# Optimization experiments

Measured on AMD Instinct MI355X. Metric: run time of the kernel, lower is better.

Reference implementation:

```python
import jax, jax.numpy as jnp
import numpy as np

N_QUBITS = 8
N_QLAYERS = 7
EPS = 1e-12


def _conv(x, w, b, stride, pad):
    y = jax.lax.conv_general_dilated(x, w, (stride, stride), [(pad, pad), (pad, pad)],
                                     dimension_numbers=("NCHW", "OIHW", "NCHW"))
    return y + b[None, :, None, None]


def _adaptive_avg_pool(x, out):
    # torch AdaptiveAvgPool2d semantics: bin i = [floor(i*H/out), ceil((i+1)*H/out))
    H, W = x.shape[-2], x.shape[-1]
    hs = [(i * H) // out for i in range(out)]
    he = [-(-((i + 1) * H) // out) for i in range(out)]
    ws = [(i * W) // out for i in range(out)]
    we = [-(-((i + 1) * W) // out) for i in range(out)]
    xh = jnp.stack([x[:, :, s:e, :].mean(axis=2) for s, e in zip(hs, he)], axis=2)
    return jnp.stack([xh[:, :, :, s:e].mean(axis=3) for s, e in zip(ws, we)], axis=3)


def _ry(st, theta, wire):
    # st: [B, 2, 2, ..., 2]; RY = [[cos, -sin], [sin, cos]] (real)
    c, s = jnp.cos(theta / 2), jnp.sin(theta / 2)
    U = jnp.stack([jnp.stack([c, -s]), jnp.stack([s, c])])  # [2,2]
    m = jnp.moveaxis(st, wire + 1, -1)
    m = m @ U.T
    return jnp.moveaxis(m, -1, wire + 1)


def _cnot(st, ctrl, tgt):
    s = jnp.moveaxis(st, (ctrl + 1, tgt + 1), (1, 2))
    s = jnp.stack([s[:, 0], jnp.flip(s[:, 1], axis=1)], axis=1)
    return jnp.moveaxis(s, (1, 2), (ctrl + 1, tgt + 1))


def _quantum(feat, q_w):
    B = feat.shape[0]
    psi = feat / jnp.maximum(jnp.linalg.norm(feat, axis=1, keepdims=True), EPS)
    st = psi.reshape((B,) + (2,) * N_QUBITS)  # wire 0 = most significant axis
    for l in range(N_QLAYERS):
        for q in range(N_QUBITS):
            st = _ry(st, q_w[l, q], q)
        for q in range(N_QUBITS - 1):
            st = _cnot(st, q, q + 1)
    s2 = st.reshape(B, 2, -1)
    return jnp.sum(s2[:, 0] ** 2, axis=-1) - jnp.sum(s2[:, 1] ** 2, axis=-1)  # [B]


def _forward(x, conv1_w, conv1_b, conv2_w, conv2_b, conv3_w, conv3_b, fc_w, fc_b, q_w,
             c1_w, c1_b, c2_w, c2_b, c3_w, c3_b, c4_w, c4_b, c5_w, c5_b):
    h = jax.nn.relu(_conv(x, conv1_w, conv1_b, 2, 2))   # [B,8,14,14]
    h = jax.nn.relu(_conv(h, conv2_w, conv2_b, 2, 1))   # [B,16,7,7]
    h = jax.nn.relu(_conv(h, conv3_w, conv3_b, 1, 1))   # [B,32,7,7]
    h = _adaptive_avg_pool(h, 3)                         # [B,32,3,3]
    h = h.reshape(h.shape[0], -1)                        # [B,288]
    feat = jax.nn.relu(h @ fc_w.T + fc_b)                # [B,256] (dropout = eval no-op)
    feat = feat / jnp.maximum(jnp.linalg.norm(feat, axis=1, keepdims=True), EPS)
    q = _quantum(feat, q_w)[:, None]                     # [B,1]
    h = jax.nn.relu(q @ c1_w.T + c1_b)
    h = jax.nn.relu(h @ c2_w.T + c2_b)
    h = jax.nn.relu(h @ c3_w.T + c3_b)
    h = jax.nn.relu(h @ c4_w.T + c4_b)
    return jax.nn.sigmoid(h @ c5_w.T + c5_b)             # [B,1]


def setup_inputs() -> dict:
    key = jax.random.key(0)
    ks = jax.random.split(key, 32)
    B = 8192
    def rn(k, shape, scale):
        return jax.random.normal(k, shape, dtype=jnp.float32) * scale
    return {
        "x": rn(ks[0], (B, 1, 28, 28), 1.0),
        "conv1_w": rn(ks[1], (8, 1, 5, 5), 0.2), "conv1_b": rn(ks[2], (8,), 0.05),
        "conv2_w": rn(ks[3], (16, 8, 3, 3), 0.12), "conv2_b": rn(ks[4], (16,), 0.05),
        "conv3_w": rn(ks[5], (32, 16, 3, 3), 0.08), "conv3_b": rn(ks[6], (32,), 0.05),
        "fc_w": rn(ks[7], (256, 288), 0.06), "fc_b": rn(ks[8], (256,), 0.02),
        "q_w": rn(ks[9], (7, 8), 1.0),
        "c1_w": rn(ks[10], (512, 1), 0.5), "c1_b": rn(ks[11], (512,), 0.02),
        "c2_w": rn(ks[12], (256, 512), 0.04), "c2_b": rn(ks[13], (256,), 0.02),
        "c3_w": rn(ks[14], (128, 256), 0.06), "c3_b": rn(ks[15], (128,), 0.02),
        "c4_w": rn(ks[16], (64, 128), 0.09), "c4_b": rn(ks[17], (64,), 0.02),
        "c5_w": rn(ks[18], (1, 64), 0.12), "c5_b": rn(ks[19], (1,), 0.02),
    }


def reference(x, conv1_w, conv1_b, conv2_w, conv2_b, conv3_w, conv3_b, fc_w, fc_b, q_w,
              c1_w, c1_b, c2_w, c2_b, c3_w, c3_b, c4_w, c4_b, c5_w, c5_b):
    return _forward(x, conv1_w, conv1_b, conv2_w, conv2_b, conv3_w, conv3_b, fc_w, fc_b, q_w,
                    c1_w, c1_b, c2_w, c2_b, c3_w, c3_b, c4_w, c4_b, c5_w, c5_b)
```

## Files before the change

kernel.cpp:

```cpp
#include <hip/hip_runtime.h>
#include <math.h>


typedef __attribute__((ext_vector_type(8))) short bf16x8;
typedef __attribute__((ext_vector_type(4))) float f32x4;

__device__ __forceinline__ unsigned rne_bf16(float x) {
  unsigned u = __float_as_uint(x);
  return (u + 0x7FFFu + ((u >> 16) & 1u)) & 0xFFFF0000u;
}

__global__ __launch_bounds__(256) void k_conv12(
    const float* __restrict__ x,
    const float* __restrict__ w1, const float* __restrict__ b1,
    const float* __restrict__ w2, const float* __restrict__ b2,
    float* __restrict__ y2p) {
  __shared__ float xin[4][784];
  __shared__ float y1p[4][8][14][20];
  __shared__ float wl1[200], bl1[8];
  __shared__ float wl2t[72][16], bl2[16];
  const int n0 = blockIdx.x * 4;
  const int tid = threadIdx.x;

  for (int i = tid; i < 200; i += 256) wl1[i] = w1[i];
  if (tid < 8) bl1[tid] = b1[tid];
  for (int i = tid; i < 1152; i += 256) {
    int k = i >> 4, co = i & 15;
    wl2t[k][co] = w2[co * 72 + k];
  }
  if (tid < 16) bl2[tid] = b2[tid];
#pragma unroll
  for (int s = 0; s < 4; ++s)
    if (tid < 196)
      reinterpret_cast<float4*>(&xin[s][0])[tid] =
          reinterpret_cast<const float4*>(&x[(size_t)(n0 + s) * 784])[tid];
  __syncthreads();

  if (tid < 224) {
    const int s = tid / 56, r = tid % 56, co = r / 7, oyh = r % 7;
    float wreg[25];
#pragma unroll
    for (int i = 0; i < 25; ++i) wreg[i] = wl1[co * 25 + i];
    const float bb = bl1[co];
#pragma unroll
    for (int half = 0; half < 2; ++half) {
      const int oy = oyh + half * 7;
      float acc[14];
#pragma unroll
      for (int ox = 0; ox < 14; ++ox) acc[ox] = bb;
#pragma unroll
      for (int ky = 0; ky < 5; ++ky) {
        const int y = oy * 2 - 2 + ky;
        if (y >= 0 && y < 28) {
          const float4* xp = reinterpret_cast<const float4*>(&xin[s][y * 28]);
          float xr[28];
#pragma unroll
          for (int v = 0; v < 7; ++v) {
            float4 q = xp[v];
            xr[v * 4 + 0] = q.x; xr[v * 4 + 1] = q.y;
            xr[v * 4 + 2] = q.z; xr[v * 4 + 3] = q.w;
          }
#pragma unroll
          for (int kx = 0; kx < 5; ++kx) {
            const float w = wreg[ky * 5 + kx];
#pragma unroll
            for (int ox = 0; ox < 14; ++ox) {
              const int xx = ox * 2 - 2 + kx;
              if (xx >= 0 && xx < 28) acc[ox] += w * xr[xx];
            }
          }
        }
      }
#pragma unroll
      for (int ox = 0; ox < 14; ++ox) y1p[s][co][oy][ox] = fmaxf(acc[ox], 0.f);
    }
  }
  __syncthreads();

  if (tid < 224) {
    const int s = tid / 56, r = tid % 56, cop = r / 7, oy = r % 7;
    const int co0 = cop * 2;
    float acc0[7], acc1[7];
#pragma unroll
    for (int ox = 0; ox < 7; ++ox) { acc0[ox] = bl2[co0]; acc1[ox] = bl2[co0 + 1]; }
    for (int ci = 0; ci < 8; ++ci) {
#pragma unroll
      for (int ky = 0; ky < 3; ++ky) {
        const int y = oy * 2 - 1 + ky;
        if (y >= 0 && y < 14) {
          const float4* rp = reinterpret_cast<const float4*>(&y1p[s][ci][y][0]);
          float4 q0 = rp[0], q1 = rp[1], q2 = rp[2], q3 = rp[3];
          float xr[14] = {q0.x, q0.y, q0.z, q0.w, q1.x, q1.y, q1.z, q1.w,
                          q2.x, q2.y, q2.z, q2.w, q3.x, q3.y};
          const int kb = ci * 9 + ky * 3;
          const float wa0 = wl2t[kb + 0][co0],     wa1 = wl2t[kb + 1][co0],     wa2 = wl2t[kb + 2][co0];
          const float wb0 = wl2t[kb + 0][co0 + 1], wb1 = wl2t[kb + 1][co0 + 1], wb2 = wl2t[kb + 2][co0 + 1];
#pragma unroll
          for (int ox = 0; ox < 7; ++ox) {
            if (2 * ox - 1 >= 0) { acc0[ox] += wa0 * xr[2 * ox - 1]; acc1[ox] += wb0 * xr[2 * ox - 1]; }
            acc0[ox] += wa1 * xr[2 * ox];
            acc1[ox] += wb1 * xr[2 * ox];
            if (2 * ox + 1 < 14) { acc0[ox] += wa2 * xr[2 * ox + 1]; acc1[ox] += wb2 * xr[2 * ox + 1]; }
          }
        }
      }
    }
    float* o0 = &y2p[(size_t)(n0 + s) * 896 + (co0 + 0) * 56 + oy * 8];
    float* o1 = &y2p[(size_t)(n0 + s) * 896 + (co0 + 1) * 56 + oy * 8];
#pragma unroll
    for (int ox = 0; ox < 7; ++ox) {
      o0[ox] = fmaxf(acc0[ox], 0.f);
      o1[ox] = fmaxf(acc1[ox], 0.f);
    }
  }
}

__global__ __launch_bounds__(256) void k_conv3pool(
    const float* __restrict__ y2p,
    const float* __restrict__ w3, const float* __restrict__ b3,
    float* __restrict__ pooled) {
  __shared__ float y2s[8][16][7][8];
  __shared__ float wl3t[144][32];
  __shared__ float bl3[32];
  const int n0 = blockIdx.x * 8;
  const int tid = threadIdx.x;

  for (int i = tid; i < 4608; i += 256) {
    int k = i >> 5, co = i & 31;
    wl3t[k][co] = w3[co * 144 + k];
  }
  if (tid < 32) bl3[tid] = b3[tid];
#pragma unroll
  for (int s = 0; s < 8; ++s)
    if (tid < 224)
      reinterpret_cast<float4*>(&y2s[s][0][0][0])[tid] =
          reinterpret_cast<const float4*>(&y2p[(size_t)(n0 + s) * 896])[tid];
  __syncthreads();

  const int s = tid >> 5, co = tid & 31;
  float acc[49];
  {
    const float bb = bl3[co];
#pragma unroll
    for (int i = 0; i < 49; ++i) acc[i] = bb;
  }
  for (int ci = 0; ci < 16; ++ci) {
    float xr[7][7];
#pragma unroll
    for (int y = 0; y < 7; ++y) {
      const float4* rp = reinterpret_cast<const float4*>(&y2s[s][ci][y][0]);
      float4 qa = rp[0], qb = rp[1];
      xr[y][0] = qa.x; xr[y][1] = qa.y; xr[y][2] = qa.z; xr[y][3] = qa.w;
      xr[y][4] = qb.x; xr[y][5] = qb.y; xr[y][6] = qb.z;
    }
    float wreg[9];
#pragma unroll
    for (int k = 0; k < 9; ++k) wreg[k] = wl3t[ci * 9 + k][co];
#pragma unroll
    for (int ky = 0; ky < 3; ++ky)
#pragma unroll
      for (int kx = 0; kx < 3; ++kx) {
        const float w = wreg[ky * 3 + kx];
#pragma unroll
        for (int oy = 0; oy < 7; ++oy) {
          const int y = oy - 1 + ky;
          if (y >= 0 && y < 7) {
#pragma unroll
            for (int ox = 0; ox < 7; ++ox) {
              const int xx = ox - 1 + kx;
              if (xx >= 0 && xx < 7) acc[oy * 7 + ox] += w * xr[y][xx];
            }
          }
        }
      }
  }
#pragma unroll
  for (int i = 0; i < 49; ++i) acc[i] = fmaxf(acc[i], 0.f);
  float* out = pooled + (size_t)(n0 + s) * 288 + co * 9;
#pragma unroll
  for (int py = 0; py < 3; ++py)
#pragma unroll
    for (int px = 0; px < 3; ++px) {
      float v = 0.f;
#pragma unroll
      for (int dy = 0; dy < 3; ++dy)
#pragma unroll
        for (int dx = 0; dx < 3; ++dx) v += acc[(2 * py + dy) * 7 + (2 * px + dx)];
      out[py * 3 + px] = v * (1.f / 9.f);
    }
}

template <int NT, int EP, bool ASYNTH>
__global__ __launch_bounds__(256) void k_rowgemm16(
    const float* __restrict__ A, const float* __restrict__ Bm,
    const float* __restrict__ bias, float* __restrict__ C,
    const float* __restrict__ sq, const float* __restrict__ sw,
    const float* __restrict__ sb, int K) {
  static_assert(NT == 128 || NT == 256, "NT");
  constexpr int NC = NT / 128;
  constexpr int NB4 = NT / 32;
  constexpr int BS = NT + 4;
  __shared__ float AT[32 * 20];
  __shared__ float BT[32 * BS];
  const int m0 = blockIdx.x * 16;
  const int tid = threadIdx.x;
  const int tr = tid >> 5, tc = tid & 31;

  float ra[2];
  float4 rb[NB4];

  auto loadAB = [&](int k0) {
#pragma unroll
    for (int e = 0; e < 2; ++e) {
      const int idx = tid + e * 256;
      const int mm = idx >> 5, kk = idx & 31;
      if (ASYNTH) ra[e] = fmaxf(sq[m0 + mm] * sw[k0 + kk] + sb[k0 + kk], 0.f);
      else ra[e] = A[(size_t)(m0 + mm) * K + k0 + kk];
    }
#pragma unroll
    for (int e = 0; e < NB4; ++e) {
      const int idx4 = tid + e * 256;
      const int nn = idx4 >> 3, kq = idx4 & 7;
      rb[e] = *reinterpret_cast<const float4*>(&Bm[(size_t)nn * K + k0 + kq * 4]);
    }
  };
  auto storeAB = [&]() {
#pragma unroll
    for (int e = 0; e < 2; ++e) {
      const int idx = tid + e * 256;
      AT[(idx & 31) * 20 + (idx >> 5)] = ra[e];
    }
#pragma unroll
    for (int e = 0; e < NB4; ++e) {
      const int idx4 = tid + e * 256;
      const int nn = idx4 >> 3, kq = idx4 & 7;
      BT[(kq * 4 + 0) * BS + nn] = rb[e].x;
      BT[(kq * 4 + 1) * BS + nn] = rb[e].y;
      BT[(kq * 4 + 2) * BS + nn] = rb[e].z;
      BT[(kq * 4 + 3) * BS + nn] = rb[e].w;
    }
  };

  float acc[2][NC][4];
#pragma unroll
  for (int i = 0; i < 2; ++i)
#pragma unroll
    for (int nc = 0; nc < NC; ++nc)
#pragma unroll
      for (int j = 0; j < 4; ++j) acc[i][nc][j] = 0.f;

  loadAB(0);
  for (int k0 = 0; k0 < K; k0 += 32) {
    __syncthreads();
    storeAB();
    __syncthreads();
    if (k0 + 32 < K) loadAB(k0 + 32);
#pragma unroll
    for (int kk = 0; kk < 32; ++kk) {
      const float2 a2 = *reinterpret_cast<const float2*>(&AT[kk * 20 + tr * 2]);
#pragma unroll
      for (int nc = 0; nc < NC; ++nc) {
        const float4 b4 = *reinterpret_cast<const float4*>(
            &BT[kk * BS + nc * 128 + tc * 4]);
        acc[0][nc][0] += a2.x * b4.x; acc[0][nc][1] += a2.x * b4.y;
        acc[0][nc][2] += a2.x * b4.z; acc[0][nc][3] += a2.x * b4.w;
        acc[1][nc][0] += a2.y * b4.x; acc[1][nc][1] += a2.y * b4.y;
        acc[1][nc][2] += a2.y * b4.z; acc[1][nc][3] += a2.y * b4.w;
      }
    }
  }

  if (EP == 2) {
    float qp[2] = {0.f, 0.f};
#pragma unroll
    for (int i = 0; i < 2; ++i)
#pragma unroll
      for (int nc = 0; nc < NC; ++nc)
#pragma unroll
        for (int j = 0; j < 4; ++j) {
          const float v = acc[i][nc][j];
          qp[i] += (nc == 0) ? v * v : -v * v;
        }
#pragma unroll
    for (int i = 0; i < 2; ++i)
#pragma unroll
      for (int d = 1; d < 32; d <<= 1) qp[i] += __shfl_xor(qp[i], d, 64);
    if (tc == 0) {
#pragma unroll
      for (int i = 0; i < 2; ++i) C[m0 + tr * 2 + i] = qp[i];
    }
  } else if (EP == 1) {
    float t[2][NC][4];
    float ss[2] = {0.f, 0.f};
#pragma unroll
    for (int i = 0; i < 2; ++i)
#pragma unroll
      for (int nc = 0; nc < NC; ++nc)
#pragma unroll
        for (int j = 0; j < 4; ++j) {
          const float v = fmaxf(acc[i][nc][j] + bias[nc * 128 + tc * 4 + j], 0.f);
          t[i][nc][j] = v;
          ss[i] += v * v;
        }
#pragma unroll
    for (int i = 0; i < 2; ++i)
#pragma unroll
      for (int d = 1; d < 32; d <<= 1) ss[i] += __shfl_xor(ss[i], d, 64);
#pragma unroll
    for (int i = 0; i < 2; ++i) {
      const float sc = 1.f / fmaxf(sqrtf(ss[i]), 1e-12f);
#pragma unroll
      for (int nc = 0; nc < NC; ++nc) {
        float4 v;
        v.x = t[i][nc][0] * sc; v.y = t[i][nc][1] * sc;
        v.z = t[i][nc][2] * sc; v.w = t[i][nc][3] * sc;
        *reinterpret_cast<float4*>(&C[(size_t)(m0 + tr * 2 + i) * NT + nc * 128 + tc * 4]) = v;
      }
    }
  } else {
#pragma unroll
    for (int i = 0; i < 2; ++i)
#pragma unroll
      for (int nc = 0; nc < NC; ++nc) {
        float4 v;
        v.x = fmaxf(acc[i][nc][0] + bias[nc * 128 + tc * 4 + 0], 0.f);
        v.y = fmaxf(acc[i][nc][1] + bias[nc * 128 + tc * 4 + 1], 0.f);
        v.z = fmaxf(acc[i][nc][2] + bias[nc * 128 + tc * 4 + 2], 0.f);
        v.w = fmaxf(acc[i][nc][3] + bias[nc * 128 + tc * 4 + 3], 0.f);
        *reinterpret_cast<float4*>(&C[(size_t)(m0 + tr * 2 + i) * NT + nc * 128 + tc * 4]) = v;
      }
  }
}

template <int NT>
__global__ __launch_bounds__(256) void k_rowgemm64(
    const float* __restrict__ A, const float* __restrict__ Bm,
    const float* __restrict__ bias, float* __restrict__ C, int K) {
  constexpr int NB = NT / 64;
  __shared__ float AT[32 * 68];
  __shared__ float BT[32 * (NT + 4)];
  constexpr int BS = NT + 4;
  const int m0 = blockIdx.x * 64;
  const int tid = threadIdx.x;
  const int tr = tid >> 4, tc = tid & 15;
  float acc[4][NB][4];
#pragma unroll
  for (int i = 0; i < 4; ++i)
#pragma unroll
    for (int nb = 0; nb < NB; ++nb)
#pragma unroll
      for (int j = 0; j < 4; ++j) acc[i][nb][j] = 0.f;

  for (int k0 = 0; k0 < K; k0 += 32) {
#pragma unroll
    for (int e = 0; e < 8; ++e) {
      int idx = tid + e * 256;
      int mm = idx >> 5, kk = idx & 31;
      AT[kk * 68 + mm] = A[(size_t)(m0 + mm) * K + k0 + kk];
    }
#pragma unroll
    for (int e = 0; e < NB * 8; ++e) {
      int idx = tid + e * 256;
      int nn = idx >> 5, kk = idx & 31;
      BT[kk * BS + nn] = Bm[(size_t)nn * K + k0 + kk];
    }
    __syncthreads();
#pragma unroll
    for (int kk = 0; kk < 32; ++kk) {
      const float4 a4 = *reinterpret_cast<const float4*>(&AT[kk * 68 + tr * 4]);
      const float a[4] = {a4.x, a4.y, a4.z, a4.w};
#pragma unroll
      for (int nb = 0; nb < NB; ++nb) {
        const float4 b4 = *reinterpret_cast<const float4*>(&BT[kk * BS + nb * 64 + tc * 4]);
        const float b[4] = {b4.x, b4.y, b4.z, b4.w};
#pragma unroll
        for (int i = 0; i < 4; ++i)
#pragma unroll
          for (int j = 0; j < 4; ++j) acc[i][nb][j] += a[i] * b[j];
      }
    }
    __syncthreads();
  }
#pragma unroll
  for (int i = 0; i < 4; ++i)
#pragma unroll
    for (int nb = 0; nb < NB; ++nb) {
      float4 v;
      v.x = fmaxf(acc[i][nb][0] + bias[nb * 64 + tc * 4 + 0], 0.f);
      v.y = fmaxf(acc[i][nb][1] + bias[nb * 64 + tc * 4 + 1], 0.f);
      v.z = fmaxf(acc[i][nb][2] + bias[nb * 64 + tc * 4 + 2], 0.f);
      v.w = fmaxf(acc[i][nb][3] + bias[nb * 64 + tc * 4 + 3], 0.f);
      *reinterpret_cast<float4*>(&C[(size_t)(m0 + tr * 4 + i) * NT + nb * 64 + tc * 4]) = v;
    }
}

__global__ __launch_bounds__(256) void k_splitW(const float* __restrict__ W,
                                                short* __restrict__ Wh,
                                                short* __restrict__ Wl, int n) {
  const int i = blockIdx.x * 256 + threadIdx.x;
  if (i < n) {
    const float x = W[i];
    const unsigned hb = rne_bf16(x);
    const float lo = x - __uint_as_float(hb);
    Wh[i] = (short)(hb >> 16);
    Wl[i] = (short)(rne_bf16(lo) >> 16);
  }
}

__global__ __launch_bounds__(64) void k_buildU(const float* __restrict__ qw,
                                               short* __restrict__ Uh,
                                               short* __restrict__ Ul) {
  const int j = blockIdx.x;
  const int t = threadIdx.x;
  float a0 = (t == j) ? 1.f : 0.f;
  float a1 = (64 + t == j) ? 1.f : 0.f;
  float a2 = (128 + t == j) ? 1.f : 0.f;
  float a3 = (192 + t == j) ? 1.f : 0.f;
  for (int l = 0; l < 7; ++l) {
#pragma unroll
    for (int q = 0; q < 8; ++q) {
      const float th = 0.5f * qw[l * 8 + q];
      const float c = cosf(th), s = sinf(th);
      const int m = 7 - q;
      if (m == 7) {
        const float n0 = c * a0 - s * a2, n2 = s * a0 + c * a2;
        const float n1 = c * a1 - s * a3, n3 = s * a1 + c * a3;
        a0 = n0; a2 = n2; a1 = n1; a3 = n3;
      } else if (m == 6) {
        const float n0 = c * a0 - s * a1, n1 = s * a0 + c * a1;
        const float n2 = c * a2 - s * a3, n3 = s * a2 + c * a3;
        a0 = n0; a1 = n1; a2 = n2; a3 = n3;
      } else {
        const float p0 = __shfl_xor(a0, 1 << m, 64);
        const float p1 = __shfl_xor(a1, 1 << m, 64);
        const float p2 = __shfl_xor(a2, 1 << m, 64);
        const float p3 = __shfl_xor(a3, 1 << m, 64);
        const float sgn = ((t >> m) & 1) ? s : -s;
        a0 = c * a0 + sgn * p0; a1 = c * a1 + sgn * p1;
        a2 = c * a2 + sgn * p2; a3 = c * a3 + sgn * p3;
      }
    }
#pragma unroll
    for (int q = 0; q < 7; ++q) {
      const int mc = 7 - q, mt = mc - 1;
      if (mc == 7) {
        const float tmp = a2; a2 = a3; a3 = tmp;
      } else if (mc == 6) {
        a1 = __shfl_xor(a1, 32, 64);
        a3 = __shfl_xor(a3, 32, 64);
      } else {
        const float p0 = __shfl_xor(a0, 1 << mt, 64);
        const float p1 = __shfl_xor(a1, 1 << mt, 64);
        const float p2 = __shfl_xor(a2, 1 << mt, 64);
        const float p3 = __shfl_xor(a3, 1 << mt, 64);
        if ((t >> mc) & 1) { a0 = p0; a1 = p1; a2 = p2; a3 = p3; }
      }
    }
  }
  const float av[4] = {a0, a1, a2, a3};
#pragma unroll
  for (int r = 0; r < 4; ++r) {
    const float x = av[r];
    const unsigned hb = rne_bf16(x);
    const float lo = x - __uint_as_float(hb);
    Uh[(r * 64 + t) * 256 + j] = (short)(hb >> 16);
    Ul[(r * 64 + t) * 256 + j] = (short)(rne_bf16(lo) >> 16);
  }
}

template <int MODE>
__global__ __launch_bounds__(256) void k_mfma16(
    const float* __restrict__ Afp, const short* __restrict__ Bh,
    const short* __restrict__ Bl, const float* __restrict__ bias,
    float* __restrict__ Cout, const float* __restrict__ sq,
    const float* __restrict__ sw, const float* __restrict__ sb, int K) {
  __shared__ float red[4][16];
  const int m0 = blockIdx.x * 16;
  const int tid = threadIdx.x;
  const int wave = tid >> 6, lane = tid & 63;
  const int lrow = lane & 15, lgrp = lane >> 4;
  const int n0 = wave * 64;

  f32x4 acc[4];
#pragma unroll
  for (int nt = 0; nt < 4; ++nt) acc[nt] = (f32x4){0.f, 0.f, 0.f, 0.f};

  float qm = 0.f;
  if (MODE == 0) qm = sq[m0 + lrow];
  const float* arow = (MODE == 1) ? (Afp + (size_t)(m0 + lrow) * K) : Afp;

  for (int k0 = 0; k0 < K; k0 += 32) {
    const int kb = k0 + lgrp * 8;
    float a[8];
    if (MODE == 0) {
      const float4 w0 = *reinterpret_cast<const float4*>(&sw[kb]);
      const float4 w1 = *reinterpret_cast<const float4*>(&sw[kb + 4]);
      const float4 b0 = *reinterpret_cast<const float4*>(&sb[kb]);
      const float4 b1 = *reinterpret_cast<const float4*>(&sb[kb + 4]);
      a[0] = fmaxf(qm * w0.x + b0.x, 0.f); a[1] = fmaxf(qm * w0.y + b0.y, 0.f);
      a[2] = fmaxf(qm * w0.z + b0.z, 0.f); a[3] = fmaxf(qm * w0.w + b0.w, 0.f);
      a[4] = fmaxf(qm * w1.x + b1.x, 0.f); a[5] = fmaxf(qm * w1.y + b1.y, 0.f);
      a[6] = fmaxf(qm * w1.z + b1.z, 0.f); a[7] = fmaxf(qm * w1.w + b1.w, 0.f);
    } else {
      const float4 a0v = *reinterpret_cast<const float4*>(&arow[kb]);
      const float4 a1v = *reinterpret_cast<const float4*>(&arow[kb + 4]);
      a[0] = a0v.x; a[1] = a0v.y; a[2] = a0v.z; a[3] = a0v.w;
      a[4] = a1v.x; a[5] = a1v.y; a[6] = a1v.z; a[7] = a1v.w;
    }
    bf16x8 ah, al;
#pragma unroll
    for (int i = 0; i < 8; ++i) {
      const unsigned hb = rne_bf16(a[i]);
      const float lo = a[i] - __uint_as_float(hb);
      ah[i] = (short)(hb >> 16);
      al[i] = (short)(rne_bf16(lo) >> 16);
    }
#pragma unroll
    for (int nt = 0; nt < 4; ++nt) {
      const size_t boff = (size_t)(n0 + nt * 16 + lrow) * K + kb;
      const bf16x8 bh = *reinterpret_cast<const bf16x8*>(&Bh[boff]);
      const bf16x8 bl = *reinterpret_cast<const bf16x8*>(&Bl[boff]);
      acc[nt] = __builtin_amdgcn_mfma_f32_16x16x32_bf16(ah, bh, acc[nt], 0, 0, 0);
      acc[nt] = __builtin_amdgcn_mfma_f32_16x16x32_bf16(ah, bl, acc[nt], 0, 0, 0);
      acc[nt] = __builtin_amdgcn_mfma_f32_16x16x32_bf16(al, bh, acc[nt], 0, 0, 0);
    }
  }

  if (MODE == 0) {
#pragma unroll
    for (int nt = 0; nt < 4; ++nt) {
      const int col = n0 + nt * 16 + lrow;
      const float bb = bias[col];
#pragma unroll
      for (int j = 0; j < 4; ++j) {
        const int row = m0 + lgrp * 4 + j;
        Cout[(size_t)row * 256 + col] = fmaxf(acc[nt][j] + bb, 0.f);
      }
    }
  } else {
    float p[4] = {0.f, 0.f, 0.f, 0.f};
#pragma unroll
    for (int nt = 0; nt < 4; ++nt)
#pragma unroll
      for (int j = 0; j < 4; ++j) { const float v = acc[nt][j]; p[j] += v * v; }
    if (wave >= 2) {
#pragma unroll
      for (int j = 0; j < 4; ++j) p[j] = -p[j];
    }
#pragma unroll
    for (int d = 1; d < 16; d <<= 1)
#pragma unroll
      for (int j = 0; j < 4; ++j) p[j] += __shfl_xor(p[j], d, 64);
    if (lrow == 0) {
#pragma unroll
      for (int j = 0; j < 4; ++j) red[wave][lgrp * 4 + j] = p[j];
    }
    __syncthreads();
    if (tid < 16)
      Cout[m0 + tid] = red[0][tid] + red[1][tid] + red[2][tid] + red[3][tid];
  }
}

__global__ __launch_bounds__(256) void k_head5(const float* __restrict__ h4,
                                               const float* __restrict__ w,
                                               const float* __restrict__ b,
                                               float* __restrict__ out) {
  const int row = blockIdx.x * 4 + (threadIdx.x >> 6);
  const int lane = threadIdx.x & 63;
  float s = h4[(size_t)row * 64 + lane] * w[lane];
#pragma unroll
  for (int d = 32; d > 0; d >>= 1) s += __shfl_xor(s, d, 64);
  if (lane == 0) out[row] = 1.f / (1.f + expf(-(s + b[0])));
}

extern "C" void kernel_launch(void* const* d_in, const int* in_sizes, int n_in,
                              void* d_out, int out_size, void* d_ws, size_t ws_size,
                              hipStream_t stream) {
  const float* x       = (const float*)d_in[0];
  const float* conv1_w = (const float*)d_in[1];
  const float* conv1_b = (const float*)d_in[2];
  const float* conv2_w = (const float*)d_in[3];
  const float* conv2_b = (const float*)d_in[4];
  const float* conv3_w = (const float*)d_in[5];
  const float* conv3_b = (const float*)d_in[6];
  const float* fc_w    = (const float*)d_in[7];
  const float* fc_b    = (const float*)d_in[8];
  const float* q_w     = (const float*)d_in[9];
  const float* c1_w    = (const float*)d_in[10];
  const float* c1_b    = (const float*)d_in[11];
  const float* c2_w    = (const float*)d_in[12];
  const float* c2_b    = (const float*)d_in[13];
  const float* c3_w    = (const float*)d_in[14];
  const float* c3_b    = (const float*)d_in[15];
  const float* c4_w    = (const float*)d_in[16];
  const float* c4_b    = (const float*)d_in[17];
  const float* c5_w    = (const float*)d_in[18];
  const float* c5_b    = (const float*)d_in[19];
  float* out = (float*)d_out;
  char* ws = (char*)d_ws;

  float* y2p    = (float*)(ws + 0);
  float* pooled = (float*)(ws + 29360128);
  short* c2h    = (short*)(ws + 38797312);
  short* c2l    = (short*)(ws + 39059456);
  float* feat   = (float*)(ws + 0);
  short* Uh     = (short*)(ws + 8388608);
  short* Ul     = (short*)(ws + 8519680);
  float* qv     = (float*)(ws + 8650752);
  float* h2     = (float*)(ws + 8683520);
  float* h3     = (float*)(ws + 17072128);
  float* h4     = (float*)(ws + 21266432);
  (void)in_sizes; (void)n_in; (void)out_size; (void)ws_size;

  k_splitW<<<512, 256, 0, stream>>>(c2_w, c2h, c2l, 256 * 512);

  k_conv12<<<2048, 256, 0, stream>>>(x, conv1_w, conv1_b, conv2_w, conv2_b, y2p);
  k_conv3pool<<<1024, 256, 0, stream>>>(y2p, conv3_w, conv3_b, pooled);
  k_rowgemm16<256, 1, false><<<512, 256, 0, stream>>>(pooled, fc_w, fc_b, feat,
                                                      nullptr, nullptr, nullptr, 288);
  k_buildU<<<256, 64, 0, stream>>>(q_w, Uh, Ul);
  k_mfma16<1><<<512, 256, 0, stream>>>(feat, Uh, Ul, nullptr, qv,
                                       nullptr, nullptr, nullptr, 256);
  k_mfma16<0><<<512, 256, 0, stream>>>(nullptr, c2h, c2l, c2_b, h2,
                                       qv, c1_w, c1_b, 512);
  k_rowgemm16<128, 0, false><<<512, 256, 0, stream>>>(h2, c3_w, c3_b, h3,
                                                      nullptr, nullptr, nullptr, 256);
  k_rowgemm64<64><<<128, 256, 0, stream>>>(h3, c4_w, c4_b, h4, 128);
  k_head5<<<2048, 256, 0, stream>>>(h4, c5_w, c5_b, out);
}
```

Measured before the change: 328.6 us.

## Move fc layer to split-bf16 MFMA and defer amplitude normalization

The fc GEMM (288->256) moves from the FP32 row-GEMM to a split-bf16 MFMA kernel. Its weights are pre-split into high and low bf16 parts. Instead of normalizing feat in place, the kernel writes partial row sums of squares, and normalization is applied later as a scalar ratio (sum of signed squares over norm squared) when building the c1 activation. All three MFMA GEMMs now use a 2-wide grid in N with 32 columns per wave, which doubles the block count to improve occupancy, at the cost of reading A twice and adding an extra weight-split launch per call.

```diff
diff --git a/kernel.cpp b/kernel.cpp
--- a/kernel.cpp
+++ b/kernel.cpp
@@ -188,6 +188,122 @@
         for (int dx = 0; dx < 3; ++dx) v += acc[(2 * py + dy) * 7 + (2 * px + dx)];
       out[py * 3 + px] = v * (1.f / 9.f);
     }
+}
+
+template <int MODE, int K>
+__global__ __launch_bounds__(256, 4) void k_mfma2(
+    const float* __restrict__ Afp, const short* __restrict__ Bh,
+    const short* __restrict__ Bl, const float* __restrict__ bias,
+    float* __restrict__ Cout, float* __restrict__ aux,
+    const float* __restrict__ qp, const float* __restrict__ rs,
+    const float* __restrict__ sw, const float* __restrict__ sb) {
+  __shared__ float red[4][16];
+  const int m0 = blockIdx.x * 16;
+  const int ny = blockIdx.y;
+  const int tid = threadIdx.x;
+  const int wave = tid >> 6, lane = tid & 63;
+  const int lrow = lane & 15, lgrp = lane >> 4;
+  const int colg = ny * 128 + wave * 32;
+
+  f32x4 acc[2];
+  acc[0] = (f32x4){0.f, 0.f, 0.f, 0.f};
+  acc[1] = (f32x4){0.f, 0.f, 0.f, 0.f};
+
+  float qm = 0.f;
+  if (MODE == 2) {
+    const int m = m0 + lrow;
+    const float num = qp[m] + qp[8192 + m];
+    const float den = fmaxf(rs[m] + rs[8192 + m], 1e-24f);
+    qm = num / den;
+  }
+  const float* arow = (MODE == 2) ? nullptr : (Afp + (size_t)(m0 + lrow) * K);
+
+#pragma unroll 4
+  for (int k0 = 0; k0 < K; k0 += 32) {
+    const int kb = k0 + lgrp * 8;
+    float a[8];
+    if (MODE == 2) {
+      const float4 w0 = *reinterpret_cast<const float4*>(&sw[kb]);
+      const float4 w1 = *reinterpret_cast<const float4*>(&sw[kb + 4]);
+      const float4 b0 = *reinterpret_cast<const float4*>(&sb[kb]);
+      const float4 b1 = *reinterpret_cast<const float4*>(&sb[kb + 4]);
+      a[0] = fmaxf(qm * w0.x + b0.x, 0.f); a[1] = fmaxf(qm * w0.y + b0.y, 0.f);
+      a[2] = fmaxf(qm * w0.z + b0.z, 0.f); a[3] = fmaxf(qm * w0.w + b0.w, 0.f);
+      a[4] = fmaxf(qm * w1.x + b1.x, 0.f); a[5] = fmaxf(qm * w1.y + b1.y, 0.f);
+      a[6] = fmaxf(qm * w1.z + b1.z, 0.f); a[7] = fmaxf(qm * w1.w + b1.w, 0.f);
+    } else {
+      const float4 a0v = *reinterpret_cast<const float4*>(&arow[kb]);
+      const float4 a1v = *reinterpret_cast<const float4*>(&arow[kb + 4]);
+      a[0] = a0v.x; a[1] = a0v.y; a[2] = a0v.z; a[3] = a0v.w;
+      a[4] = a1v.x; a[5] = a1v.y; a[6] = a1v.z; a[7] = a1v.w;
+    }
+    bf16x8 ah, al;
+#pragma unroll
+    for (int i = 0; i < 8; ++i) {
+      const unsigned hb = rne_bf16(a[i]);
+      const float lo = a[i] - __uint_as_float(hb);
+      ah[i] = (short)(hb >> 16);
+      al[i] = (short)(rne_bf16(lo) >> 16);
+    }
+#pragma unroll
+    for (int nt = 0; nt < 2; ++nt) {
+      const size_t boff = (size_t)(colg + nt * 16 + lrow) * K + kb;
+      const bf16x8 bh = *reinterpret_cast<const bf16x8*>(&Bh[boff]);
+      const bf16x8 bl = *reinterpret_cast<const bf16x8*>(&Bl[boff]);
+      acc[nt] = __builtin_amdgcn_mfma_f32_16x16x32_bf16(ah, bh, acc[nt], 0, 0, 0);
+      acc[nt] = __builtin_amdgcn_mfma_f32_16x16x32_bf16(ah, bl, acc[nt], 0, 0, 0);
+      acc[nt] = __builtin_amdgcn_mfma_f32_16x16x32_bf16(al, bh, acc[nt], 0, 0, 0);
+    }
+  }
+
+  if (MODE == 1) {
+    float p[4] = {0.f, 0.f, 0.f, 0.f};
+#pragma unroll
+    for (int nt = 0; nt < 2; ++nt)
+#pragma unroll
+      for (int j = 0; j < 4; ++j) { const float v = acc[nt][j]; p[j] += v * v; }
+#pragma unroll
+    for (int d = 1; d < 16; d <<= 1)
+#pragma unroll
+      for (int j = 0; j < 4; ++j) p[j] += __shfl_xor(p[j], d, 64);
+    if (lrow == 0) {
+#pragma unroll
+      for (int j = 0; j < 4; ++j) red[wave][lgrp * 4 + j] = p[j];
+    }
+    __syncthreads();
+    if (tid < 16) {
+      const float v = red[0][tid] + red[1][tid] + red[2][tid] + red[3][tid];
+      Cout[ny * 8192 + m0 + tid] = ny ? -v : v;
+    }
+  } else {
+    float p[4] = {0.f, 0.f, 0.f, 0.f};
+#pragma unroll
+    for (int nt = 0; nt < 2; ++nt) {
+      const int col = colg + nt * 16 + lrow;
+      const float bb = bias[col];
+#pragma unroll
+      for (int j = 0; j < 4; ++j) {
+        const int row = m0 + lgrp * 4 + j;
+        const float v = fmaxf(acc[nt][j] + bb, 0.f);
+        Cout[(size_t)row * 256 + col] = v;
+        if (MODE == 0) p[j] += v * v;
+      }
+    }
+    if (MODE == 0) {
+#pragma unroll
+      for (int d = 1; d < 16; d <<= 1)
+#pragma unroll
+        for (int j = 0; j < 4; ++j) p[j] += __shfl_xor(p[j], d, 64);
+      if (lrow == 0) {
+#pragma unroll
+        for (int j = 0; j < 4; ++j) red[wave][lgrp * 4 + j] = p[j];
+      }
+      __syncthreads();
+      if (tid < 16)
+        aux[ny * 8192 + m0 + tid] =
+            red[0][tid] + red[1][tid] + red[2][tid] + red[3][tid];
+    }
+  }
 }
 
 template <int NT, int EP, bool ASYNTH>
@@ -270,66 +386,17 @@
     }
   }
 
-  if (EP == 2) {
-    float qp[2] = {0.f, 0.f};
-#pragma unroll
-    for (int i = 0; i < 2; ++i)
-#pragma unroll
-      for (int nc = 0; nc < NC; ++nc)
-#pragma unroll
-        for (int j = 0; j < 4; ++j) {
-          const float v = acc[i][nc][j];
-          qp[i] += (nc == 0) ? v * v : -v * v;
-        }
-#pragma unroll
-    for (int i = 0; i < 2; ++i)
-#pragma unroll
-      for (int d = 1; d < 32; d <<= 1) qp[i] += __shfl_xor(qp[i], d, 64);
-    if (tc == 0) {
-#pragma unroll
-      for (int i = 0; i < 2; ++i) C[m0 + tr * 2 + i] = qp[i];
-    }
-  } else if (EP == 1) {
-    float t[2][NC][4];
-    float ss[2] = {0.f, 0.f};
-#pragma unroll
-    for (int i = 0; i < 2; ++i)
-#pragma unroll
-      for (int nc = 0; nc < NC; ++nc)
-#pragma unroll
-        for (int j = 0; j < 4; ++j) {
-          const float v = fmaxf(acc[i][nc][j] + bias[nc * 128 + tc * 4 + j], 0.f);
-          t[i][nc][j] = v;
-          ss[i] += v * v;
-        }
-#pragma unroll
-    for (int i = 0; i < 2; ++i)
-#pragma unroll
-      for (int d = 1; d < 32; d <<= 1) ss[i] += __shfl_xor(ss[i], d, 64);
-#pragma unroll
-    for (int i = 0; i < 2; ++i) {
-      const float sc = 1.f / fmaxf(sqrtf(ss[i]), 1e-12f);
-#pragma unroll
-      for (int nc = 0; nc < NC; ++nc) {
-        float4 v;
-        v.x = t[i][nc][0] * sc; v.y = t[i][nc][1] * sc;
-        v.z = t[i][nc][2] * sc; v.w = t[i][nc][3] * sc;
-        *reinterpret_cast<float4*>(&C[(size_t)(m0 + tr * 2 + i) * NT + nc * 128 + tc * 4]) = v;
-      }
-    }
-  } else {
-#pragma unroll
-    for (int i = 0; i < 2; ++i)
-#pragma unroll
-      for (int nc = 0; nc < NC; ++nc) {
-        float4 v;
-        v.x = fmaxf(acc[i][nc][0] + bias[nc * 128 + tc * 4 + 0], 0.f);
-        v.y = fmaxf(acc[i][nc][1] + bias[nc * 128 + tc * 4 + 1], 0.f);
-        v.z = fmaxf(acc[i][nc][2] + bias[nc * 128 + tc * 4 + 2], 0.f);
-        v.w = fmaxf(acc[i][nc][3] + bias[nc * 128 + tc * 4 + 3], 0.f);
-        *reinterpret_cast<float4*>(&C[(size_t)(m0 + tr * 2 + i) * NT + nc * 128 + tc * 4]) = v;
-      }
-  }
+#pragma unroll
+  for (int i = 0; i < 2; ++i)
+#pragma unroll
+    for (int nc = 0; nc < NC; ++nc) {
+      float4 v;
+      v.x = fmaxf(acc[i][nc][0] + bias[nc * 128 + tc * 4 + 0], 0.f);
+      v.y = fmaxf(acc[i][nc][1] + bias[nc * 128 + tc * 4 + 1], 0.f);
+      v.z = fmaxf(acc[i][nc][2] + bias[nc * 128 + tc * 4 + 2], 0.f);
+      v.w = fmaxf(acc[i][nc][3] + bias[nc * 128 + tc * 4 + 3], 0.f);
+      *reinterpret_cast<float4*>(&C[(size_t)(m0 + tr * 2 + i) * NT + nc * 128 + tc * 4]) = v;
+    }
 }
 
 template <int NT>
@@ -465,99 +532,6 @@
     const float lo = x - __uint_as_float(hb);
     Uh[(r * 64 + t) * 256 + j] = (short)(hb >> 16);
     Ul[(r * 64 + t) * 256 + j] = (short)(rne_bf16(lo) >> 16);
-  }
-}
-
-template <int MODE>
-__global__ __launch_bounds__(256) void k_mfma16(
-    const float* __restrict__ Afp, const short* __restrict__ Bh,
-    const short* __restrict__ Bl, const float* __restrict__ bias,
-    float* __restrict__ Cout, const float* __restrict__ sq,
-    const float* __restrict__ sw, const float* __restrict__ sb, int K) {
-  __shared__ float red[4][16];
-  const int m0 = blockIdx.x * 16;
-  const int tid = threadIdx.x;
-  const int wave = tid >> 6, lane = tid & 63;
-  const int lrow = lane & 15, lgrp = lane >> 4;
-  const int n0 = wave * 64;
-
-  f32x4 acc[4];
-#pragma unroll
-  for (int nt = 0; nt < 4; ++nt) acc[nt] = (f32x4){0.f, 0.f, 0.f, 0.f};
-
-  float qm = 0.f;
-  if (MODE == 0) qm = sq[m0 + lrow];
-  const float* arow = (MODE == 1) ? (Afp + (size_t)(m0 + lrow) * K) : Afp;
-
-  for (int k0 = 0; k0 < K; k0 += 32) {
-    const int kb = k0 + lgrp * 8;
-    float a[8];
-    if (MODE == 0) {
-      const float4 w0 = *reinterpret_cast<const float4*>(&sw[kb]);
-      const float4 w1 = *reinterpret_cast<const float4*>(&sw[kb + 4]);
-      const float4 b0 = *reinterpret_cast<const float4*>(&sb[kb]);
-      const float4 b1 = *reinterpret_cast<const float4*>(&sb[kb + 4]);
-      a[0] = fmaxf(qm * w0.x + b0.x, 0.f); a[1] = fmaxf(qm * w0.y + b0.y, 0.f);
-      a[2] = fmaxf(qm * w0.z + b0.z, 0.f); a[3] = fmaxf(qm * w0.w + b0.w, 0.f);
-      a[4] = fmaxf(qm * w1.x + b1.x, 0.f); a[5] = fmaxf(qm * w1.y + b1.y, 0.f);
-      a[6] = fmaxf(qm * w1.z + b1.z, 0.f); a[7] = fmaxf(qm * w1.w + b1.w, 0.f);
-    } else {
-      const float4 a0v = *reinterpret_cast<const float4*>(&arow[kb]);
-      const float4 a1v = *reinterpret_cast<const float4*>(&arow[kb + 4]);
-      a[0] = a0v.x; a[1] = a0v.y; a[2] = a0v.z; a[3] = a0v.w;
-      a[4] = a1v.x; a[5] = a1v.y; a[6] = a1v.z; a[7] = a1v.w;
-    }
-    bf16x8 ah, al;
-#pragma unroll
-    for (int i = 0; i < 8; ++i) {
-      const unsigned hb = rne_bf16(a[i]);
-      const float lo = a[i] - __uint_as_float(hb);
-      ah[i] = (short)(hb >> 16);
-      al[i] = (short)(rne_bf16(lo) >> 16);
-    }
-#pragma unroll
-    for (int nt = 0; nt < 4; ++nt) {
-      const size_t boff = (size_t)(n0 + nt * 16 + lrow) * K + kb;
-      const bf16x8 bh = *reinterpret_cast<const bf16x8*>(&Bh[boff]);
-      const bf16x8 bl = *reinterpret_cast<const bf16x8*>(&Bl[boff]);
-      acc[nt] = __builtin_amdgcn_mfma_f32_16x16x32_bf16(ah, bh, acc[nt], 0, 0, 0);
-      acc[nt] = __builtin_amdgcn_mfma_f32_16x16x32_bf16(ah, bl, acc[nt], 0, 0, 0);
-      acc[nt] = __builtin_amdgcn_mfma_f32_16x16x32_bf16(al, bh, acc[nt], 0, 0, 0);
-    }
-  }
-
-  if (MODE == 0) {
-#pragma unroll
-    for (int nt = 0; nt < 4; ++nt) {
-      const int col = n0 + nt * 16 + lrow;
-      const float bb = bias[col];
-#pragma unroll
-      for (int j = 0; j < 4; ++j) {
-        const int row = m0 + lgrp * 4 + j;
-        Cout[(size_t)row * 256 + col] = fmaxf(acc[nt][j] + bb, 0.f);
-      }
-    }
-  } else {
-    float p[4] = {0.f, 0.f, 0.f, 0.f};
-#pragma unroll
-    for (int nt = 0; nt < 4; ++nt)
-#pragma unroll
-      for (int j = 0; j < 4; ++j) { const float v = acc[nt][j]; p[j] += v * v; }
-    if (wave >= 2) {
-#pragma unroll
-      for (int j = 0; j < 4; ++j) p[j] = -p[j];
-    }
-#pragma unroll
-    for (int d = 1; d < 16; d <<= 1)
-#pragma unroll
-      for (int j = 0; j < 4; ++j) p[j] += __shfl_xor(p[j], d, 64);
-    if (lrow == 0) {
-#pragma unroll
-      for (int j = 0; j < 4; ++j) red[wave][lgrp * 4 + j] = p[j];
-    }
-    __syncthreads();
-    if (tid < 16)
-      Cout[m0 + tid] = red[0][tid] + red[1][tid] + red[2][tid] + red[3][tid];
   }
 }
 
@@ -603,26 +577,32 @@
   float* pooled = (float*)(ws + 29360128);
   short* c2h    = (short*)(ws + 38797312);
   short* c2l    = (short*)(ws + 39059456);
+  short* fch    = (short*)(ws + 39321600);
+  short* fcl    = (short*)(ws + 39469056);
   float* feat   = (float*)(ws + 0);
   short* Uh     = (short*)(ws + 8388608);
   short* Ul     = (short*)(ws + 8519680);
-  float* qv     = (float*)(ws + 8650752);
-  float* h2     = (float*)(ws + 8683520);
-  float* h3     = (float*)(ws + 17072128);
-  float* h4     = (float*)(ws + 21266432);
+  float* qpb    = (float*)(ws + 8650752);
+  float* rsb    = (float*)(ws + 8716288);
+  float* h2     = (float*)(ws + 8781824);
+  float* h3     = (float*)(ws + 17170432);
+  float* h4     = (float*)(ws + 21364736);
   (void)in_sizes; (void)n_in; (void)out_size; (void)ws_size;
 
   k_splitW<<<512, 256, 0, stream>>>(c2_w, c2h, c2l, 256 * 512);
+  k_splitW<<<288, 256, 0, stream>>>(fc_w, fch, fcl, 256 * 288);
 
   k_conv12<<<2048, 256, 0, stream>>>(x, conv1_w, conv1_b, conv2_w, conv2_b, y2p);
   k_conv3pool<<<1024, 256, 0, stream>>>(y2p, conv3_w, conv3_b, pooled);
-  k_rowgemm16<256, 1, false><<<512, 256, 0, stream>>>(pooled, fc_w, fc_b, feat,
-                                                      nullptr, nullptr, nullptr, 288);
+
+  dim3 g2(512, 2);
+  k_mfma2<0, 288><<<g2, 256, 0, stream>>>(pooled, fch, fcl, fc_b, feat, rsb,
+                                          nullptr, nullptr, nullptr, nullptr);
   k_buildU<<<256, 64, 0, stream>>>(q_w, Uh, Ul);
-  k_mfma16<1><<<512, 256, 0, stream>>>(feat, Uh, Ul, nullptr, qv,
-                                       nullptr, nullptr, nullptr, 256);
-  k_mfma16<0><<<512, 256, 0, stream>>>(nullptr, c2h, c2l, c2_b, h2,
-                                       qv, c1_w, c1_b, 512);
+  k_mfma2<1, 256><<<g2, 256, 0, stream>>>(feat, Uh, Ul, nullptr, qpb, nullptr,
+                                          nullptr, nullptr, nullptr, nullptr);
+  k_mfma2<2, 512><<<g2, 256, 0, stream>>>(nullptr, c2h, c2l, c2_b, h2, nullptr,
+                                          qpb, rsb, c1_w, c1_b);
   k_rowgemm16<128, 0, false><<<512, 256, 0, stream>>>(h2, c3_w, c3_b, h3,
                                                       nullptr, nullptr, nullptr, 256);
   k_rowgemm64<64><<<128, 256, 0, stream>>>(h3, c4_w, c4_b, h4, 128);
```

Result: no change. 324.5 us (-1.2%).
